# Kernel tuning notes

Hardware: AMD Instinct MI355X
Metric: run time of the kernel (lower is better)

The kernel has to match this reference:

```python
import jax, jax.numpy as jnp
from jax import lax
import numpy as np

B, C, H, W = 32, 256, 56, 56
R = max(1, C // 16)  # reduced channels = 16
K = 7                # spatial kernel


def setup_inputs() -> dict:
    key = jax.random.key(0)
    k_x, k1, k2, k3 = jax.random.split(key, 4)
    x = jax.random.normal(k_x, (B, C, H, W), dtype=jnp.float32)
    # shared MLP 1x1 convs (bias=False): stored as 2D matrices
    w1 = jax.random.normal(k1, (R, C), dtype=jnp.float32) * (1.0 / np.sqrt(C))
    w2 = jax.random.normal(k2, (C, R), dtype=jnp.float32) * (1.0 / np.sqrt(R))
    # spatial 7x7 conv: 2 in-channels (avg,max) -> 1 out, OIHW
    w_sp = jax.random.normal(k3, (1, 2, K, K), dtype=jnp.float32) * (1.0 / np.sqrt(2 * K * K))
    return {"x": x, "w1": w1, "w2": w2, "w_sp": w_sp}


def reference(x, w1, w2, w_sp):
    # ---- Channel attention ----
    avg = jnp.mean(x, axis=(2, 3))            # (B, C)
    mx = jnp.max(x, axis=(2, 3))              # (B, C)

    def mlp(v):  # shared 1x1-conv MLP on pooled vectors
        return jnp.einsum('cr,br->bc', w2, jax.nn.relu(jnp.einsum('rc,bc->br', w1, v)))

    ca = jax.nn.sigmoid(mlp(avg) + mlp(mx))[:, :, None, None]  # (B, C, 1, 1)
    xc = x * ca                                # (B, C, H, W)

    # ---- Spatial attention ----
    pooled = jnp.stack([jnp.mean(xc, axis=1), jnp.max(xc, axis=1)], axis=1)  # (B, 2, H, W)
    pad = (K - 1) // 2
    sa = jax.nn.sigmoid(
        lax.conv_general_dilated(pooled, w_sp, window_strides=(1, 1),
                                 padding=[(pad, pad), (pad, pad)],
                                 dimension_numbers=('NCHW', 'OIHW', 'NCHW')))  # (B, 1, H, W)

    # ---- Residual ----
    return x + xc * sa
```

## Files before the change

kernel.cpp:

```cpp
#include <hip/hip_runtime.h>
#include <math.h>

#define B_ 32
#define C_ 256
#define H_ 56
#define W_ 56
#define HW_ (H_*W_)
#define Q_ (HW_/4)
#define R_ 16
#define K_ 7

__device__ __forceinline__ float sigmoidf_(float v) { return 1.0f / (1.0f + expf(-v)); }

__global__ void k_pool_bc(const float* __restrict__ x,
                          float* __restrict__ avg, float* __restrict__ mx) {
    const int bc = blockIdx.x;
    const float4* xp = (const float4*)(x + (size_t)bc * HW_);
    float s = 0.0f, m = -INFINITY;
    for (int i = threadIdx.x; i < Q_; i += blockDim.x) {
        float4 v = xp[i];
        s += v.x + v.y + v.z + v.w;
        m = fmaxf(m, fmaxf(fmaxf(v.x, v.y), fmaxf(v.z, v.w)));
    }
    #pragma unroll
    for (int off = 32; off > 0; off >>= 1) {
        s += __shfl_down(s, off, 64);
        m  = fmaxf(m, __shfl_down(m, off, 64));
    }
    __shared__ float ss[4], sm[4];
    const int wave = threadIdx.x >> 6;
    if ((threadIdx.x & 63) == 0) { ss[wave] = s; sm[wave] = m; }
    __syncthreads();
    if (threadIdx.x == 0) {
        float S = ss[0] + ss[1] + ss[2] + ss[3];
        float M = fmaxf(fmaxf(sm[0], sm[1]), fmaxf(sm[2], sm[3]));
        avg[bc] = S * (1.0f / HW_);
        mx[bc]  = M;
    }
}

__global__ void k_mlp_ca(const float* __restrict__ avg, const float* __restrict__ mx,
                         const float* __restrict__ w1, const float* __restrict__ w2,
                         float* __restrict__ ca) {
    const int b = blockIdx.x;
    __shared__ float sa_[C_], sm_[C_], h_[R_];
    const int t = threadIdx.x;
    sa_[t] = avg[b * C_ + t];
    sm_[t] = mx[b * C_ + t];
    __syncthreads();
    if (t < R_) {
        float ha = 0.0f, hm = 0.0f;
        for (int c = 0; c < C_; ++c) {
            const float wv = w1[t * C_ + c];
            ha += wv * sa_[c];
            hm += wv * sm_[c];
        }
        h_[t] = fmaxf(ha, 0.0f) + fmaxf(hm, 0.0f);
    }
    __syncthreads();
    float acc = 0.0f;
    #pragma unroll
    for (int r = 0; r < R_; ++r) acc += w2[t * R_ + r] * h_[r];
    ca[b * C_ + t] = sigmoidf_(acc);
}

__global__ void __launch_bounds__(256)
k_spatial_pool(const float* __restrict__ x, const float* __restrict__ ca,
               float* __restrict__ pooled) {
    const int b  = blockIdx.y;
    const int q0 = blockIdx.x * 16;
    const int t  = threadIdx.x;
    const int tq = t & 15;
    const int tc = t >> 4;
    const int q  = q0 + tq;

    const float4* xp = (const float4*)(x + (size_t)b * C_ * HW_);
    const float* cab = ca + b * C_;

    float4 s = {0.f, 0.f, 0.f, 0.f};
    float4 m = {-INFINITY, -INFINITY, -INFINITY, -INFINITY};
    #pragma unroll 4
    for (int i = 0; i < 16; ++i) {
        const int c = tc * 16 + i;
        const float a = cab[c];
        float4 v = xp[(size_t)c * Q_ + q];
        v.x *= a; v.y *= a; v.z *= a; v.w *= a;
        s.x += v.x; s.y += v.y; s.z += v.z; s.w += v.w;
        m.x = fmaxf(m.x, v.x); m.y = fmaxf(m.y, v.y);
        m.z = fmaxf(m.z, v.z); m.w = fmaxf(m.w, v.w);
    }

    __shared__ float4 ls[256];
    __shared__ float4 lm[256];
    ls[t] = s; lm[t] = m;
    __syncthreads();
    #pragma unroll
    for (int st = 8; st >= 1; st >>= 1) {
        if (tc < st) {
            const int o = t + st * 16;
            float4 os = ls[o], om = lm[o];
            s.x += os.x; s.y += os.y; s.z += os.z; s.w += os.w;
            m.x = fmaxf(m.x, om.x); m.y = fmaxf(m.y, om.y);
            m.z = fmaxf(m.z, om.z); m.w = fmaxf(m.w, om.w);
            ls[t] = s; lm[t] = m;
        }
        __syncthreads();
    }
    if (tc == 0) {
        const float inv = 1.0f / C_;
        float4 sm4 = {s.x * inv, s.y * inv, s.z * inv, s.w * inv};
        ((float4*)(pooled + (size_t)b * 2 * HW_))[q]       = sm4;
        ((float4*)(pooled + (size_t)b * 2 * HW_ + HW_))[q] = m;
    }
}

__global__ void k_conv_sa(const float* __restrict__ pooled, const float* __restrict__ wsp,
                          float* __restrict__ sa) {
    __shared__ float wv[2 * K_ * K_];
    if (threadIdx.x < 2 * K_ * K_) wv[threadIdx.x] = wsp[threadIdx.x];
    __syncthreads();
    const int idx = blockIdx.x * blockDim.x + threadIdx.x;
    if (idx >= B_ * HW_) return;
    const int b = idx / HW_;
    const int hw = idx % HW_;
    const int h = hw / W_, w = hw % W_;
    const float* pa = pooled + (size_t)b * 2 * HW_;
    const float* pm = pa + HW_;
    float acc = 0.0f;
    #pragma unroll
    for (int ky = 0; ky < K_; ++ky) {
        const int y = h + ky - 3;
        if (y < 0 || y >= H_) continue;
        #pragma unroll
        for (int kx = 0; kx < K_; ++kx) {
            const int xx = w + kx - 3;
            if (xx < 0 || xx >= W_) continue;
            const int o = y * W_ + xx;
            acc += wv[ky * K_ + kx] * pa[o] + wv[K_ * K_ + ky * K_ + kx] * pm[o];
        }
    }
    sa[idx] = sigmoidf_(acc);
}

__global__ void k_finalize(const float* __restrict__ x, const float* __restrict__ ca,
                           const float* __restrict__ sa, float* __restrict__ out) {
    const size_t idx = (size_t)blockIdx.x * blockDim.x + threadIdx.x;
    if (idx >= (size_t)B_ * C_ * Q_) return;
    const size_t e = idx * 4;
    const int b  = (int)(e / ((size_t)C_ * HW_));
    const int c  = (int)((e / HW_) % C_);
    const int hw = (int)(e % HW_);
    const float a = ca[b * C_ + c];
    const float4 s4 = *(const float4*)(sa + (size_t)b * HW_ + hw);
    const float4 v  = *(const float4*)(x + e);
    float4 o;
    o.x = v.x * (1.0f + a * s4.x);
    o.y = v.y * (1.0f + a * s4.y);
    o.z = v.z * (1.0f + a * s4.z);
    o.w = v.w * (1.0f + a * s4.w);
    *(float4*)((float*)out + e) = o;
}

extern "C" void kernel_launch(void* const* d_in, const int* in_sizes, int n_in,
                              void* d_out, int out_size, void* d_ws, size_t ws_size,
                              hipStream_t stream) {
    const float* x   = (const float*)d_in[0];
    const float* w1  = (const float*)d_in[1];
    const float* w2  = (const float*)d_in[2];
    const float* wsp = (const float*)d_in[3];
    float* out = (float*)d_out;

    float* ws     = (float*)d_ws;
    float* avg    = ws;
    float* mx     = avg + B_ * C_;
    float* ca     = mx + B_ * C_;
    float* pooled = ca + B_ * C_;
    float* sa     = pooled + (size_t)B_ * 2 * HW_;

    k_pool_bc<<<B_ * C_, 256, 0, stream>>>(x, avg, mx);
    k_mlp_ca<<<B_, C_, 0, stream>>>(avg, mx, w1, w2, ca);
    {
        dim3 g(Q_ / 16, B_);
        k_spatial_pool<<<g, 256, 0, stream>>>(x, ca, pooled);
    }
    {
        const int n = B_ * HW_;
        k_conv_sa<<<(n + 255) / 256, 256, 0, stream>>>(pooled, wsp, sa);
    }
    {
        const size_t n = (size_t)B_ * C_ * Q_;
        k_finalize<<<(int)((n + 255) / 256), 256, 0, stream>>>(x, ca, sa, out);
    }
}
```

Baseline: 231.9 us.

## Fuse CBAM stages into one cooperative kernel with grid syncs and nontemporal stores

Replaces the five separate launches with one cooperative persistent kernel of 1024 blocks that runs channel pooling, the MLP, spatial pooling, the 7x7 conv and the finalize step in order, separated by grid.sync(). The channel-pool and finalize stages now give each wave a whole channel map instead of using a block per map or a flat index. The output is written with nontemporal stores and the sigmoid uses __expf. The aim is to remove launch gaps and write-cache pollution. In exchange it pays for four grid-wide barriers, relies on all 1024 blocks being co-resident, and falls back to the old path if the cooperative launch fails.

```diff
diff --git a/kernel.cpp b/kernel.cpp
--- a/kernel.cpp
+++ b/kernel.cpp
@@ -1,5 +1,8 @@
 #include <hip/hip_runtime.h>
+#include <hip/hip_cooperative_groups.h>
 #include <math.h>
+
+namespace cg = cooperative_groups;
 
 #define B_ 32
 #define C_ 256
@@ -9,8 +12,191 @@
 #define Q_ (HW_/4)
 #define R_ 16
 #define K_ 7
-
-__device__ __forceinline__ float sigmoidf_(float v) { return 1.0f / (1.0f + expf(-v)); }
+#define NBLK 1024
+
+typedef float nat_f4 __attribute__((ext_vector_type(4)));
+
+__device__ __forceinline__ float sigmoidf_(float v) { return 1.0f / (1.0f + __expf(-v)); }
+
+__device__ __forceinline__ void nt_store4(float4 v, float4* p) {
+    nat_f4 nv;
+    nv.x = v.x; nv.y = v.y; nv.z = v.z; nv.w = v.w;
+    __builtin_nontemporal_store(nv, (nat_f4*)p);
+}
+
+__global__ void __launch_bounds__(256, 4)
+k_cbam_fused(const float* __restrict__ x, const float* __restrict__ w1,
+             const float* __restrict__ w2, const float* __restrict__ wsp,
+             float* __restrict__ avg, float* __restrict__ mxv, float* __restrict__ ca,
+             float* __restrict__ pooled, float* __restrict__ sa, float* __restrict__ out) {
+    cg::grid_group grid = cg::this_grid();
+    const int tid  = threadIdx.x;
+    const int lane = tid & 63;
+    const int wave = tid >> 6;
+
+    __shared__ float4 ls[256];
+    __shared__ float4 lm[256];
+    __shared__ float  sA[C_], sM[C_], hh[R_];
+    __shared__ float  wconv[2 * K_ * K_];
+
+    {
+        const int nw = gridDim.x << 2;
+        for (int map = (blockIdx.x << 2) + wave; map < B_ * C_; map += nw) {
+            const float4* xp = (const float4*)(x + (size_t)map * HW_);
+            float s = 0.0f, m = -INFINITY;
+            #pragma unroll
+            for (int k = 0; k < 12; ++k) {
+                float4 v = xp[(k << 6) + lane];
+                s += v.x + v.y + v.z + v.w;
+                m = fmaxf(m, fmaxf(fmaxf(v.x, v.y), fmaxf(v.z, v.w)));
+            }
+            if (lane < 16) {
+                float4 v = xp[768 + lane];
+                s += v.x + v.y + v.z + v.w;
+                m = fmaxf(m, fmaxf(fmaxf(v.x, v.y), fmaxf(v.z, v.w)));
+            }
+            #pragma unroll
+            for (int off = 32; off > 0; off >>= 1) {
+                s += __shfl_xor(s, off, 64);
+                m = fmaxf(m, __shfl_xor(m, off, 64));
+            }
+            if (lane == 0) {
+                avg[map] = s * (1.0f / HW_);
+                mxv[map] = m;
+            }
+        }
+    }
+    grid.sync();
+
+    if (blockIdx.x < B_) {
+        const int b = blockIdx.x;
+        sA[tid] = avg[b * C_ + tid];
+        sM[tid] = mxv[b * C_ + tid];
+        __syncthreads();
+        if (tid < R_) {
+            float ha = 0.0f, hm = 0.0f;
+            for (int c = 0; c < C_; ++c) {
+                const float wv = w1[tid * C_ + c];
+                ha += wv * sA[c];
+                hm += wv * sM[c];
+            }
+            hh[tid] = fmaxf(ha, 0.0f) + fmaxf(hm, 0.0f);
+        }
+        __syncthreads();
+        float acc = 0.0f;
+        #pragma unroll
+        for (int r = 0; r < R_; ++r) acc += w2[tid * R_ + r] * hh[r];
+        ca[b * C_ + tid] = sigmoidf_(acc);
+    }
+    grid.sync();
+
+    {
+        const int tq = tid & 15;
+        const int tc = tid >> 4;
+        for (int u = blockIdx.x; u < B_ * 49; u += gridDim.x) {
+            const int b  = u / 49;
+            const int q0 = (u - b * 49) << 4;
+            const int q  = q0 + tq;
+            const float4* xp = (const float4*)(x + (size_t)b * C_ * HW_);
+            const float* cab = ca + b * C_;
+
+            float4 s = {0.f, 0.f, 0.f, 0.f};
+            float4 m = {-INFINITY, -INFINITY, -INFINITY, -INFINITY};
+            #pragma unroll 4
+            for (int i = 0; i < 16; ++i) {
+                const int c = (tc << 4) + i;
+                const float a = cab[c];
+                float4 v = xp[(size_t)c * Q_ + q];
+                v.x *= a; v.y *= a; v.z *= a; v.w *= a;
+                s.x += v.x; s.y += v.y; s.z += v.z; s.w += v.w;
+                m.x = fmaxf(m.x, v.x); m.y = fmaxf(m.y, v.y);
+                m.z = fmaxf(m.z, v.z); m.w = fmaxf(m.w, v.w);
+            }
+            ls[tid] = s; lm[tid] = m;
+            __syncthreads();
+            #pragma unroll
+            for (int st = 8; st >= 1; st >>= 1) {
+                if (tc < st) {
+                    const int o = tid + st * 16;
+                    float4 os = ls[o], om = lm[o];
+                    s.x += os.x; s.y += os.y; s.z += os.z; s.w += os.w;
+                    m.x = fmaxf(m.x, om.x); m.y = fmaxf(m.y, om.y);
+                    m.z = fmaxf(m.z, om.z); m.w = fmaxf(m.w, om.w);
+                    ls[tid] = s; lm[tid] = m;
+                }
+                __syncthreads();
+            }
+            if (tc == 0) {
+                const float inv = 1.0f / C_;
+                float4 sm4 = {s.x * inv, s.y * inv, s.z * inv, s.w * inv};
+                ((float4*)(pooled + (size_t)b * 2 * HW_))[q]       = sm4;
+                ((float4*)(pooled + (size_t)b * 2 * HW_ + HW_))[q] = m;
+            }
+            __syncthreads();
+        }
+    }
+    grid.sync();
+
+    {
+        if (tid < 2 * K_ * K_) wconv[tid] = wsp[tid];
+        __syncthreads();
+        const int idx = blockIdx.x * blockDim.x + tid;
+        if (idx < B_ * HW_) {
+            const int b  = idx / HW_;
+            const int hw = idx % HW_;
+            const int h = hw / W_, w = hw % W_;
+            const float* pa = pooled + (size_t)b * 2 * HW_;
+            const float* pm = pa + HW_;
+            float acc = 0.0f;
+            #pragma unroll
+            for (int ky = 0; ky < K_; ++ky) {
+                const int y = h + ky - 3;
+                if (y < 0 || y >= H_) continue;
+                #pragma unroll
+                for (int kx = 0; kx < K_; ++kx) {
+                    const int xx = w + kx - 3;
+                    if (xx < 0 || xx >= W_) continue;
+                    const int o = y * W_ + xx;
+                    acc += wconv[ky * K_ + kx] * pa[o] + wconv[K_ * K_ + ky * K_ + kx] * pm[o];
+                }
+            }
+            sa[idx] = sigmoidf_(acc);
+        }
+    }
+    grid.sync();
+
+    {
+        const int nw = gridDim.x << 2;
+        for (int map = (blockIdx.x << 2) + wave; map < B_ * C_; map += nw) {
+            const int b = map >> 8;
+            const float a = ca[map];
+            const float4* xp = (const float4*)(x  + (size_t)map * HW_);
+            const float4* sp = (const float4*)(sa + (size_t)b * HW_);
+            float4* op = (float4*)(out + (size_t)map * HW_);
+            #pragma unroll
+            for (int k = 0; k < 12; ++k) {
+                const int q = (k << 6) + lane;
+                float4 v = xp[q], t = sp[q];
+                float4 o;
+                o.x = v.x * (1.0f + a * t.x);
+                o.y = v.y * (1.0f + a * t.y);
+                o.z = v.z * (1.0f + a * t.z);
+                o.w = v.w * (1.0f + a * t.w);
+                nt_store4(o, op + q);
+            }
+            if (lane < 16) {
+                const int q = 768 + lane;
+                float4 v = xp[q], t = sp[q];
+                float4 o;
+                o.x = v.x * (1.0f + a * t.x);
+                o.y = v.y * (1.0f + a * t.y);
+                o.z = v.z * (1.0f + a * t.z);
+                o.w = v.w * (1.0f + a * t.w);
+                nt_store4(o, op + q);
+            }
+        }
+    }
+}
 
 __global__ void k_pool_bc(const float* __restrict__ x,
                           float* __restrict__ avg, float* __restrict__ mx) {
@@ -177,18 +363,19 @@
     float* pooled = ca + B_ * C_;
     float* sa     = pooled + (size_t)B_ * 2 * HW_;
 
-    k_pool_bc<<<B_ * C_, 256, 0, stream>>>(x, avg, mx);
-    k_mlp_ca<<<B_, C_, 0, stream>>>(avg, mx, w1, w2, ca);
-    {
+    void* args[] = {(void*)&x, (void*)&w1, (void*)&w2, (void*)&wsp,
+                    (void*)&avg, (void*)&mx, (void*)&ca,
+                    (void*)&pooled, (void*)&sa, (void*)&out};
+    hipError_t err = hipLaunchCooperativeKernel((const void*)k_cbam_fused,
+                                                dim3(NBLK), dim3(256), args, 0, stream);
+    if (err != hipSuccess) {
+        k_pool_bc<<<B_ * C_, 256, 0, stream>>>(x, avg, mx);
+        k_mlp_ca<<<B_, C_, 0, stream>>>(avg, mx, w1, w2, ca);
         dim3 g(Q_ / 16, B_);
         k_spatial_pool<<<g, 256, 0, stream>>>(x, ca, pooled);
-    }
-    {
         const int n = B_ * HW_;
         k_conv_sa<<<(n + 255) / 256, 256, 0, stream>>>(pooled, wsp, sa);
-    }
-    {
-        const size_t n = (size_t)B_ * C_ * Q_;
-        k_finalize<<<(int)((n + 255) / 256), 256, 0, stream>>>(x, ca, sa, out);
-    }
-}
+        const size_t nf = (size_t)B_ * C_ * Q_;
+        k_finalize<<<(int)((nf + 255) / 256), 256, 0, stream>>>(x, ca, sa, out);
+    }
+}
```

Result: slower. 680.4 us (+193.5%).

## Fuse channel pooling with MLP and spatial conv with finalize, add nontemporal stores

Applied to the files above, without the earlier changes.

Merges per-map pooling and the channel MLP into one kernel, in which the last block per batch (found with an atomic counter) computes the channel attention. It also fuses the 7x7 spatial conv into the final elementwise kernel, using a shared-memory halo tile over two rows, so the sa buffer round trip and two launches go away. Output writes use nontemporal stores, and pooling assigns one wave per map. This adds a memset and atomic synchronization, and each finalize block recomputes the conv for its own rows.

```diff
diff --git a/kernel.cpp b/kernel.cpp
--- a/kernel.cpp
+++ b/kernel.cpp
@@ -10,58 +10,85 @@
 #define R_ 16
 #define K_ 7
 
-__device__ __forceinline__ float sigmoidf_(float v) { return 1.0f / (1.0f + expf(-v)); }
-
-__global__ void k_pool_bc(const float* __restrict__ x,
-                          float* __restrict__ avg, float* __restrict__ mx) {
-    const int bc = blockIdx.x;
-    const float4* xp = (const float4*)(x + (size_t)bc * HW_);
-    float s = 0.0f, m = -INFINITY;
-    for (int i = threadIdx.x; i < Q_; i += blockDim.x) {
-        float4 v = xp[i];
-        s += v.x + v.y + v.z + v.w;
-        m = fmaxf(m, fmaxf(fmaxf(v.x, v.y), fmaxf(v.z, v.w)));
-    }
-    #pragma unroll
-    for (int off = 32; off > 0; off >>= 1) {
-        s += __shfl_down(s, off, 64);
-        m  = fmaxf(m, __shfl_down(m, off, 64));
-    }
-    __shared__ float ss[4], sm[4];
-    const int wave = threadIdx.x >> 6;
-    if ((threadIdx.x & 63) == 0) { ss[wave] = s; sm[wave] = m; }
-    __syncthreads();
-    if (threadIdx.x == 0) {
-        float S = ss[0] + ss[1] + ss[2] + ss[3];
-        float M = fmaxf(fmaxf(sm[0], sm[1]), fmaxf(sm[2], sm[3]));
-        avg[bc] = S * (1.0f / HW_);
-        mx[bc]  = M;
-    }
-}
-
-__global__ void k_mlp_ca(const float* __restrict__ avg, const float* __restrict__ mx,
-                         const float* __restrict__ w1, const float* __restrict__ w2,
-                         float* __restrict__ ca) {
-    const int b = blockIdx.x;
-    __shared__ float sa_[C_], sm_[C_], h_[R_];
-    const int t = threadIdx.x;
-    sa_[t] = avg[b * C_ + t];
-    sm_[t] = mx[b * C_ + t];
-    __syncthreads();
-    if (t < R_) {
-        float ha = 0.0f, hm = 0.0f;
-        for (int c = 0; c < C_; ++c) {
-            const float wv = w1[t * C_ + c];
-            ha += wv * sa_[c];
-            hm += wv * sm_[c];
-        }
-        h_[t] = fmaxf(ha, 0.0f) + fmaxf(hm, 0.0f);
-    }
-    __syncthreads();
-    float acc = 0.0f;
-    #pragma unroll
-    for (int r = 0; r < R_; ++r) acc += w2[t * R_ + r] * h_[r];
-    ca[b * C_ + t] = sigmoidf_(acc);
+typedef float nat_f4 __attribute__((ext_vector_type(4)));
+
+__device__ __forceinline__ float sigmoidf_(float v) { return 1.0f / (1.0f + __expf(-v)); }
+
+__device__ __forceinline__ void nt_store4(float4 v, float4* p) {
+    nat_f4 nv;
+    nv.x = v.x; nv.y = v.y; nv.z = v.z; nv.w = v.w;
+    __builtin_nontemporal_store(nv, (nat_f4*)p);
+}
+
+__global__ void __launch_bounds__(256)
+k_pool_mlp(const float* __restrict__ x, const float* __restrict__ w1,
+           const float* __restrict__ w2, float* __restrict__ avg,
+           float* __restrict__ mxv, float* __restrict__ ca,
+           unsigned* __restrict__ done) {
+    const int tid  = threadIdx.x;
+    const int lane = tid & 63;
+    const int wave = tid >> 6;
+    const int map  = (blockIdx.x << 2) + wave;
+    const int b    = blockIdx.x >> 6;
+
+    {
+        const float4* xp = (const float4*)(x + (size_t)map * HW_);
+        float s = 0.0f, m = -INFINITY;
+        #pragma unroll
+        for (int k = 0; k < 12; ++k) {
+            float4 v = xp[(k << 6) + lane];
+            s += v.x + v.y + v.z + v.w;
+            m = fmaxf(m, fmaxf(fmaxf(v.x, v.y), fmaxf(v.z, v.w)));
+        }
+        if (lane < 16) {
+            float4 v = xp[768 + lane];
+            s += v.x + v.y + v.z + v.w;
+            m = fmaxf(m, fmaxf(fmaxf(v.x, v.y), fmaxf(v.z, v.w)));
+        }
+        #pragma unroll
+        for (int off = 32; off > 0; off >>= 1) {
+            s += __shfl_xor(s, off, 64);
+            m = fmaxf(m, __shfl_xor(m, off, 64));
+        }
+        if (lane == 0) {
+            __hip_atomic_store(&avg[map], s * (1.0f / HW_),
+                               __ATOMIC_RELEASE, __HIP_MEMORY_SCOPE_AGENT);
+            __hip_atomic_store(&mxv[map], m,
+                               __ATOMIC_RELEASE, __HIP_MEMORY_SCOPE_AGENT);
+        }
+    }
+
+    __shared__ int isLast;
+    __syncthreads();
+    if (tid == 0) {
+        __threadfence();
+        unsigned old = atomicAdd(done + b, 1u);
+        isLast = (old == 63u);
+    }
+    __syncthreads();
+
+    if (isLast) {
+        __shared__ float sA[C_], sM[C_], hh[R_];
+        sA[tid] = __hip_atomic_load(&avg[b * C_ + tid],
+                                    __ATOMIC_ACQUIRE, __HIP_MEMORY_SCOPE_AGENT);
+        sM[tid] = __hip_atomic_load(&mxv[b * C_ + tid],
+                                    __ATOMIC_ACQUIRE, __HIP_MEMORY_SCOPE_AGENT);
+        __syncthreads();
+        if (tid < R_) {
+            float ha = 0.0f, hm = 0.0f;
+            for (int c = 0; c < C_; ++c) {
+                const float wv = w1[tid * C_ + c];
+                ha += wv * sA[c];
+                hm += wv * sM[c];
+            }
+            hh[tid] = fmaxf(ha, 0.0f) + fmaxf(hm, 0.0f);
+        }
+        __syncthreads();
+        float acc = 0.0f;
+        #pragma unroll
+        for (int r = 0; r < R_; ++r) acc += w2[tid * R_ + r] * hh[r];
+        ca[b * C_ + tid] = sigmoidf_(acc);
+    }
 }
 
 __global__ void __launch_bounds__(256)
@@ -114,51 +141,73 @@
     }
 }
 
-__global__ void k_conv_sa(const float* __restrict__ pooled, const float* __restrict__ wsp,
-                          float* __restrict__ sa) {
-    __shared__ float wv[2 * K_ * K_];
-    if (threadIdx.x < 2 * K_ * K_) wv[threadIdx.x] = wsp[threadIdx.x];
-    __syncthreads();
-    const int idx = blockIdx.x * blockDim.x + threadIdx.x;
-    if (idx >= B_ * HW_) return;
-    const int b = idx / HW_;
-    const int hw = idx % HW_;
-    const int h = hw / W_, w = hw % W_;
-    const float* pa = pooled + (size_t)b * 2 * HW_;
-    const float* pm = pa + HW_;
-    float acc = 0.0f;
-    #pragma unroll
-    for (int ky = 0; ky < K_; ++ky) {
-        const int y = h + ky - 3;
-        if (y < 0 || y >= H_) continue;
-        #pragma unroll
-        for (int kx = 0; kx < K_; ++kx) {
-            const int xx = w + kx - 3;
-            if (xx < 0 || xx >= W_) continue;
-            const int o = y * W_ + xx;
-            acc += wv[ky * K_ + kx] * pa[o] + wv[K_ * K_ + ky * K_ + kx] * pm[o];
-        }
-    }
-    sa[idx] = sigmoidf_(acc);
-}
-
-__global__ void k_finalize(const float* __restrict__ x, const float* __restrict__ ca,
-                           const float* __restrict__ sa, float* __restrict__ out) {
-    const size_t idx = (size_t)blockIdx.x * blockDim.x + threadIdx.x;
-    if (idx >= (size_t)B_ * C_ * Q_) return;
-    const size_t e = idx * 4;
-    const int b  = (int)(e / ((size_t)C_ * HW_));
-    const int c  = (int)((e / HW_) % C_);
-    const int hw = (int)(e % HW_);
-    const float a = ca[b * C_ + c];
-    const float4 s4 = *(const float4*)(sa + (size_t)b * HW_ + hw);
-    const float4 v  = *(const float4*)(x + e);
-    float4 o;
-    o.x = v.x * (1.0f + a * s4.x);
-    o.y = v.y * (1.0f + a * s4.y);
-    o.z = v.z * (1.0f + a * s4.z);
-    o.w = v.w * (1.0f + a * s4.w);
-    *(float4*)((float*)out + e) = o;
+__global__ void __launch_bounds__(256)
+k_conv_finalize(const float* __restrict__ x, const float* __restrict__ pooled,
+                const float* __restrict__ wsp, const float* __restrict__ ca,
+                float* __restrict__ out) {
+    const int b   = blockIdx.y;
+    const int r0  = blockIdx.x * 2;
+    const int tid = threadIdx.x;
+
+    __shared__ float PH[2][8][62];
+    __shared__ __align__(16) float ssa[112];
+    __shared__ float sca[C_];
+    __shared__ float wc[2 * K_ * K_];
+
+    if (tid < 2 * K_ * K_) wc[tid] = wsp[tid];
+    sca[tid] = ca[b * C_ + tid];
+
+    for (int idx = tid; idx < 992; idx += 256) {
+        const int plane = idx / 496;
+        const int rem   = idx - plane * 496;
+        const int lr    = rem / 62;
+        const int cpad  = rem - lr * 62;
+        const int row   = r0 - 3 + lr;
+        const int col   = cpad - 3;
+        float v = 0.0f;
+        if (row >= 0 && row < H_ && col >= 0 && col < W_)
+            v = pooled[((size_t)b * 2 + plane) * HW_ + row * W_ + col];
+        PH[plane][lr][cpad] = v;
+    }
+    __syncthreads();
+
+    if (tid < 112) {
+        const int prow = tid / 56;
+        const int pcol = tid - prow * 56;
+        float acc = 0.0f;
+        #pragma unroll
+        for (int ky = 0; ky < K_; ++ky) {
+            #pragma unroll
+            for (int kx = 0; kx < K_; ++kx) {
+                acc += wc[ky * K_ + kx]          * PH[0][prow + ky][pcol + kx]
+                     + wc[49 + ky * K_ + kx]     * PH[1][prow + ky][pcol + kx];
+            }
+        }
+        ssa[tid] = sigmoidf_(acc);
+    }
+    __syncthreads();
+
+    const int cg   = tid >> 5;
+    const int lane = tid & 31;
+    if (lane < 28) {
+        const float4* xb = (const float4*)(x + (size_t)b * C_ * HW_);
+        float4* ob = (float4*)(out + (size_t)b * C_ * HW_);
+        const int base = r0 * 14;
+        const float4 s4 = ((const float4*)ssa)[lane];
+        #pragma unroll 4
+        for (int g = 0; g < 32; ++g) {
+            const int c = (g << 3) + cg;
+            const float a = sca[c];
+            const size_t o = (size_t)c * Q_ + base + lane;
+            float4 v = xb[o];
+            float4 r;
+            r.x = v.x * (1.0f + a * s4.x);
+            r.y = v.y * (1.0f + a * s4.y);
+            r.z = v.z * (1.0f + a * s4.z);
+            r.w = v.w * (1.0f + a * s4.w);
+            nt_store4(r, ob + o);
+        }
+    }
 }
 
 extern "C" void kernel_launch(void* const* d_in, const int* in_sizes, int n_in,
@@ -175,20 +224,20 @@
     float* mx     = avg + B_ * C_;
     float* ca     = mx + B_ * C_;
     float* pooled = ca + B_ * C_;
-    float* sa     = pooled + (size_t)B_ * 2 * HW_;
-
-    k_pool_bc<<<B_ * C_, 256, 0, stream>>>(x, avg, mx);
-    k_mlp_ca<<<B_, C_, 0, stream>>>(avg, mx, w1, w2, ca);
+    float* sa_ws  = pooled + (size_t)B_ * 2 * HW_;
+    unsigned* done = (unsigned*)(sa_ws + (size_t)B_ * HW_);
+
+    hipMemsetAsync((void*)done, 0, B_ * sizeof(unsigned), stream);
+
+    k_pool_mlp<<<(B_ * C_) / 4, 256, 0, stream>>>(x, w1, w2, avg, mx, ca, done);
+
     {
         dim3 g(Q_ / 16, B_);
         k_spatial_pool<<<g, 256, 0, stream>>>(x, ca, pooled);
     }
+
     {
-        const int n = B_ * HW_;
-        k_conv_sa<<<(n + 255) / 256, 256, 0, stream>>>(pooled, wsp, sa);
-    }
-    {
-        const size_t n = (size_t)B_ * C_ * Q_;
-        k_finalize<<<(int)((n + 255) / 256), 256, 0, stream>>>(x, ca, sa, out);
-    }
-}
+        dim3 g(H_ / 2, B_);
+        k_conv_finalize<<<g, 256, 0, stream>>>(x, pooled, wsp, ca, out);
+    }
+}
```

New measurement: 718.8 us. +210.0%, slower.
